# Optimization experiments

Hardware: AMD Instinct MI355X
Metric: run time of the kernel (lower is better)

## Reference

```python
import jax, jax.numpy as jnp
import numpy as np


def _proj(W, b, x):
    # 1x1 conv == per-pixel GEMM over channels: [O,C] x [B,C,H,W] -> [B,O,H,W]
    return jnp.einsum('oc,bchw->bohw', W, x) + b[None, :, None, None]


def _cross(src, ctx, Wq, bq, Wk, bk, Wv, bv):
    # queries from src, keys/values from ctx; returns [B,C,H,W]
    B, C, H, W = src.shape
    HW = H * W
    q = _proj(Wq, bq, src).reshape(B, -1, HW)   # [B, C//8, HW]
    k = _proj(Wk, bk, ctx).reshape(B, -1, HW)   # [B, C//8, HW]
    v = _proj(Wv, bv, ctx).reshape(B, C, HW)    # [B, C,    HW]
    # attn[b,i,j] = softmax_j( q[b,:,i] . k[b,:,j] )
    attn = jax.nn.softmax(jnp.einsum('bci,bcj->bij', q, k), axis=-1)
    out = jnp.einsum('bcj,bij->bci', v, attn)   # [B, C, HW]
    return out.reshape(B, C, H, W)


def setup_inputs() -> dict:
    key = jax.random.key(0)
    ks = jax.random.split(key, 8)
    dim = 256
    B, H, W = 4, 64, 64
    return {
        'x': jax.random.normal(ks[0], (B, dim, H, W), jnp.float32),
        'y': jax.random.normal(ks[1], (B, dim, H, W), jnp.float32),
        'Wq': jax.random.normal(ks[2], (dim // 8, dim), jnp.float32) * 0.05,
        'bq': jax.random.normal(ks[3], (dim // 8,), jnp.float32) * 0.05,
        'Wk': jax.random.normal(ks[4], (dim // 8, dim), jnp.float32) * 0.05,
        'bk': jax.random.normal(ks[5], (dim // 8,), jnp.float32) * 0.05,
        'Wv': jax.random.normal(ks[6], (dim, dim), jnp.float32) * 0.05,
        'bv': jax.random.normal(ks[7], (dim,), jnp.float32) * 0.05,
    }


def reference(x, y, Wq, bq, Wk, bk, Wv, bv):
    outx = _cross(x, y, Wq, bq, Wk, bk, Wv, bv)  # x queries attend to y
    outy = _cross(y, x, Wq, bq, Wk, bk, Wv, bv)  # y queries attend to x
    return (outx, outy)
```

## Files before the change

### kernel.cpp

```cpp
#include <hip/hip_runtime.h>

#define BB 4
#define CC 256
#define DD 32
#define SS 4096

typedef __bf16 bf16;
typedef __bf16 bf16x8 __attribute__((ext_vector_type(8)));
typedef __bf16 bf16x4 __attribute__((ext_vector_type(4)));
typedef float f32x4 __attribute__((ext_vector_type(4)));
typedef unsigned int u32;
typedef u32 u32x4 __attribute__((ext_vector_type(4)));
typedef unsigned short u16;

#define Q_OFF  0
#define K_OFF  1048576
#define V_OFF  2097152
#define WB_OFF 10485760
#define CH_ELEM 16384

static __device__ __forceinline__ u32 pack2(float lo, float hi) {
    bf16 a = (bf16)lo, b = (bf16)hi;
    u16 ua = __builtin_bit_cast(u16, a), ub = __builtin_bit_cast(u16, b);
    return (u32)ua | ((u32)ub << 16);
}

static __device__ __forceinline__ void bar_lds() {
    asm volatile("s_waitcnt lgkmcnt(0)" ::: "memory");
    __builtin_amdgcn_s_barrier();
    asm volatile("" ::: "memory");
}

static __device__ __forceinline__ void bar_vm12() {
    asm volatile("s_waitcnt vmcnt(12)" ::: "memory");
    __builtin_amdgcn_s_barrier();
    asm volatile("" ::: "memory");
}
static __device__ __forceinline__ void bar_plain() {
    asm volatile("" ::: "memory");
    __builtin_amdgcn_s_barrier();
    asm volatile("" ::: "memory");
}

__global__ __launch_bounds__(256) void convert_w_kernel(
    const float* __restrict__ Wq, const float* __restrict__ Wk,
    const float* __restrict__ Wv, bf16* __restrict__ wb)
{
    const int gid = blockIdx.x*256 + threadIdx.x;
    const int idx = gid*8;
    const int o = idx >> 8, cc = idx & 255;
    const float* row = (o < 32) ? (Wq + (size_t)o*CC)
                     : (o < 64) ? (Wk + (size_t)(o-32)*CC)
                                : (Wv + (size_t)(o-64)*CC);
    const float4 a = *(const float4*)(row + cc);
    const float4 c = *(const float4*)(row + cc + 4);
    bf16x8 pk;
    pk[0]=(bf16)a.x; pk[1]=(bf16)a.y; pk[2]=(bf16)a.z; pk[3]=(bf16)a.w;
    pk[4]=(bf16)c.x; pk[5]=(bf16)c.y; pk[6]=(bf16)c.z; pk[7]=(bf16)c.w;
    *(bf16x8*)(wb + idx) = pk;
}

__global__ __launch_bounds__(256, 2) void proj_all_kernel(
    const float* __restrict__ x, const float* __restrict__ y,
    const bf16* __restrict__ wb,
    const float* __restrict__ bq, const float* __restrict__ bk,
    const float* __restrict__ bv,
    bf16* __restrict__ qout, bf16* __restrict__ kout, bf16* __restrict__ vout)
{
    __shared__ __align__(16) char smem[2*5120];
    bf16* xT  = (bf16*)smem;
    u32*  xTw = (u32*)smem;

    const int t    = threadIdx.x;
    const int lane = t & 63;
    const int w    = t >> 6;
    const int ln   = lane & 15;
    const int quad = lane >> 4;

    const int bid  = blockIdx.x;
    const int dirb = bid & 7;
    const int src  = dirb >> 2;
    const int b    = dirb & 3;
    const int i0   = (bid >> 3) * 64;
    const float* in = src ? y : x;
    const float* xbase = in + (size_t)b*CC*SS + i0;

    const int cp = t >> 4;
    const int pq = (t & 15) * 4;

    float bias[5];
    #pragma unroll
    for (int nbl = 0; nbl < 5; ++nbl) {
        const int o = 80*w + nbl*16 + ln;
        bias[nbl] = (o < 32) ? bq[o] : (o < 64) ? bk[o-32] : bv[o-64];
    }
    f32x4 acc[4][5];
    #pragma unroll
    for (int mb = 0; mb < 4; ++mb)
        #pragma unroll
        for (int nbl = 0; nbl < 5; ++nbl)
            acc[mb][nbl] = (f32x4){bias[nbl], bias[nbl], bias[nbl], bias[nbl]};

    const bf16* wrow = wb + (size_t)(80*w + ln)*CC + quad*8;
    bf16x8 bf[5];
    #pragma unroll
    for (int nbl = 0; nbl < 5; ++nbl)
        bf[nbl] = *(const bf16x8*)(wrow + (size_t)nbl*16*CC);

    {
        const float* r0 = xbase + (size_t)(2*cp)*SS + pq;
        const float4 a0 = *(const float4*)r0;
        const float4 a1 = *(const float4*)(r0 + SS);
        xTw[(pq+0)*20 + cp] = pack2(a0.x, a1.x);
        xTw[(pq+1)*20 + cp] = pack2(a0.y, a1.y);
        xTw[(pq+2)*20 + cp] = pack2(a0.z, a1.z);
        xTw[(pq+3)*20 + cp] = pack2(a0.w, a1.w);
    }
    float4 a0, a1;
    {
        const float* r1 = xbase + (size_t)(32 + 2*cp)*SS + pq;
        a0 = *(const float4*)r1;
        a1 = *(const float4*)(r1 + SS);
    }
    bar_lds();

    for (int n = 0; n < 8; ++n) {
        bf16x8 af[4];
        #pragma unroll
        for (int mb = 0; mb < 4; ++mb)
            af[mb] = *(const bf16x8*)(xT + (n&1)*2560 + (mb*16 + ln)*40 + quad*8);
        if (n < 7) {
            u32* dst = xTw + ((n+1)&1)*1280;
            dst[(pq+0)*20 + cp] = pack2(a0.x, a1.x);
            dst[(pq+1)*20 + cp] = pack2(a0.y, a1.y);
            dst[(pq+2)*20 + cp] = pack2(a0.z, a1.z);
            dst[(pq+3)*20 + cp] = pack2(a0.w, a1.w);
        }
        {
            const int cc2 = ((n+2)*32) & 255;
            const float* r2 = xbase + (size_t)(cc2 + 2*cp)*SS + pq;
            a0 = *(const float4*)r2;
            a1 = *(const float4*)(r2 + SS);
        }
        #pragma unroll
        for (int mb = 0; mb < 4; ++mb)
            #pragma unroll
            for (int nbl = 0; nbl < 5; ++nbl)
                acc[mb][nbl] = __builtin_amdgcn_mfma_f32_16x16x32_bf16(
                                   af[mb], bf[nbl], acc[mb][nbl], 0, 0, 0);
        const int ccn = ((n+1)*32) & 255;
        #pragma unroll
        for (int nbl = 0; nbl < 5; ++nbl)
            bf[nbl] = *(const bf16x8*)(wrow + (size_t)nbl*16*CC + ccn);
        bar_lds();
    }

    bf16* qo = qout + (size_t)(src*BB + b)*SS*DD;
    bf16* ko = kout + (size_t)(src*BB + b)*SS*DD;
    bf16* vo = vout + (size_t)(src*BB + b)*CC*SS;
    const int n0 = i0 >> 6;
    #pragma unroll
    for (int nbl = 0; nbl < 5; ++nbl) {
        const int o = 80*w + nbl*16 + ln;
        if (o < 32) {
            #pragma unroll
            for (int mb = 0; mb < 4; ++mb)
                #pragma unroll
                for (int r = 0; r < 4; ++r)
                    qo[(size_t)(i0 + mb*16 + quad*4 + r)*DD + o] = (bf16)acc[mb][nbl][r];
        } else if (o < 64) {
            #pragma unroll
            for (int mb = 0; mb < 4; ++mb)
                #pragma unroll
                for (int r = 0; r < 4; ++r)
                    ko[(size_t)(i0 + mb*16 + quad*4 + r)*DD + (o-32)] = (bf16)acc[mb][nbl][r];
        } else {
            const int c = o - 64;
            const int cb = c >> 4, cl = c & 15;
            #pragma unroll
            for (int mb = 0; mb < 4; ++mb) {
                bf16x4 pk;
                #pragma unroll
                for (int r = 0; r < 4; ++r) pk[r] = (bf16)acc[mb][nbl][r];
                *(bf16x4*)(vo + (size_t)(2*n0 + (mb>>1))*8192 + cb*512
                              + (quad*16 + cl)*8 + (mb&1)*4) = pk;
            }
        }
    }
}

#define L2E   1.4426950408889634f
#define SM_C  (16.0f * L2E)

__global__ __launch_bounds__(256, 2) void attn_kernel(
    const bf16* __restrict__ qg, const bf16* __restrict__ kg,
    const bf16* __restrict__ vg, float* __restrict__ out)
{
    __shared__ __align__(16) char vsm[2*32768];

    const int t    = threadIdx.x;
    const int lane = t & 63;
    const int w    = t >> 6;
    const int ln   = lane & 15;
    const int quad = lane >> 4;

    const int bid  = blockIdx.x;
    const int dirb = bid & 7;
    const int dir  = dirb >> 2;
    const int b    = dirb & 3;
    const int i0   = (bid >> 3) * 64;

    const bf16* q = qg + ((size_t)dir*BB + b)*SS*DD;
    const bf16* k = kg + ((size_t)(1-dir)*BB + b)*SS*DD;
    const bf16* v = vg + ((size_t)(1-dir)*BB + b)*(size_t)CC*SS;
    float* op = out + ((size_t)dir*BB + b)*(size_t)CC*SS;

    const bf16x8 bq = *(const bf16x8*)(q + (size_t)(i0 + w*16 + ln)*DD + quad*8);
    const bf16* kbase = k + (size_t)ln*DD + quad*8;
    const bf16* vstage = v + w*512 + lane*8;
    char* lds0 = vsm + w*1024;

    f32x4 o[16];
    #pragma unroll
    for (int cb = 0; cb < 16; ++cb) o[cb] = (f32x4){0.f,0.f,0.f,0.f};
    f32x4 lpq = (f32x4){0.f,0.f,0.f,0.f};

    bf16x8 kf[4];
    #pragma unroll
    for (int nb = 0; nb < 4; ++nb)
        kf[nb] = *(const bf16x8*)(kbase + (size_t)(nb*16)*DD);

    #define STAGE(ch, buf) do {                                               \
        const bf16* gp_ = vstage + (size_t)(ch)*CH_ELEM;                      \
        char* lp_ = lds0 + (buf)*32768;                                       \
        _Pragma("unroll")                                                     \
        for (int j = 0; j < 8; ++j)                                           \
            __builtin_amdgcn_global_load_lds(                                 \
                (const __attribute__((address_space(1))) void*)(gp_ + j*2048),\
                (__attribute__((address_space(3))) void*)(lp_ + j*4096),      \
                16, 0, 0);                                                    \
    } while (0)

    #define SMAX(sarr, pa) do {                                               \
        float e_[4][4];                                                       \
        _Pragma("unroll")                                                     \
        for (int nb = 0; nb < 4; ++nb)                                        \
            _Pragma("unroll")                                                 \
            for (int r = 0; r < 4; ++r) {                                     \
                e_[nb][r] = exp2f((sarr)[nb][r]*L2E - SM_C);                   \
                lpq[r] += e_[nb][r];                                          \
            }                                                                 \
        _Pragma("unroll")                                                     \
        for (int ks = 0; ks < 2; ++ks) {                                      \
            u32x4 pk_;                                                        \
            _Pragma("unroll")                                                 \
            for (int jp = 0; jp < 4; ++jp)                                    \
                pk_[jp] = pack2(e_[2*ks + (jp>>1)][2*(jp&1)],                 \
                                e_[2*ks + (jp>>1)][2*(jp&1) + 1]);            \
            (pa)[ks] = __builtin_bit_cast(bf16x8, pk_);                       \
        }                                                                     \
    } while (0)

    bf16x8 paA[2], paB[2];
    {
        f32x4 s[4];
        #pragma unroll
        for (int nb = 0; nb < 4; ++nb)
            s[nb] = __builtin_amdgcn_mfma_f32_16x16x32_bf16(
                        kf[nb], bq, (f32x4){0.f,0.f,0.f,0.f}, 0, 0, 0);
        STAGE(0, 0);
        STAGE(1, 1);
        #pragma unroll
        for (int nb = 0; nb < 4; ++nb)
            kf[nb] = *(const bf16x8*)(kbase + (size_t)(64 + nb*16)*DD);
        SMAX(s, paA);
    }

    for (int n = 0; n < 64; ++n) {
        if (n < 63) {
            f32x4 s[4];
            #pragma unroll
            for (int nb = 0; nb < 4; ++nb)
                s[nb] = __builtin_amdgcn_mfma_f32_16x16x32_bf16(
                            kf[nb], bq, (f32x4){0.f,0.f,0.f,0.f}, 0, 0, 0);
            const int j2 = ((n + 2) & 63) * 64;
            #pragma unroll
            for (int nb = 0; nb < 4; ++nb)
                kf[nb] = *(const bf16x8*)(kbase + (size_t)(j2 + nb*16)*DD);
            SMAX(s, paB);
        }

        bar_vm12();

        const char* bufp = vsm + (n & 1)*32768;
        __builtin_amdgcn_s_setprio(1);
        #pragma unroll
        for (int st = 0; st < 32; ++st) {
            const int cb = st & 15;
            const bf16x8 vfr = *(const bf16x8*)(bufp + st*1024 + lane*16);
            o[cb] = __builtin_amdgcn_mfma_f32_16x16x32_bf16(
                        paA[st >> 4], vfr, o[cb], 0, 0, 0);
        }
        __builtin_amdgcn_s_setprio(0);

        bar_plain();
        STAGE((n + 2) & 63, n & 1);

        paA[0] = paB[0];
        paA[1] = paB[1];
    }

    float lp = (lpq[0] + lpq[1]) + (lpq[2] + lpq[3]);
    lp += __shfl_xor(lp, 16);
    lp += __shfl_xor(lp, 32);
    f32x4 ri;
    #pragma unroll
    for (int r = 0; r < 4; ++r)
        ri[r] = 1.0f / __shfl(lp, quad*4 + r);

    #pragma unroll
    for (int cb = 0; cb < 16; ++cb) {
        const int c = cb*16 + ln;
        float4 val = make_float4(o[cb][0]*ri[0], o[cb][1]*ri[1],
                                 o[cb][2]*ri[2], o[cb][3]*ri[3]);
        *(float4*)(op + (size_t)c*SS + i0 + w*16 + quad*4) = val;
    }
    #undef STAGE
    #undef SMAX
}

extern "C" void kernel_launch(void* const* d_in, const int* in_sizes, int n_in,
                              void* d_out, int out_size, void* d_ws, size_t ws_size,
                              hipStream_t stream)
{
    const float* x  = (const float*)d_in[0];
    const float* y  = (const float*)d_in[1];
    const float* Wq = (const float*)d_in[2];
    const float* bq = (const float*)d_in[3];
    const float* Wk = (const float*)d_in[4];
    const float* bk = (const float*)d_in[5];
    const float* Wv = (const float*)d_in[6];
    const float* bv = (const float*)d_in[7];
    float* out = (float*)d_out;
    bf16* ws   = (bf16*)d_ws;

    bf16* qw = ws + Q_OFF;
    bf16* kw = ws + K_OFF;
    bf16* vw = ws + V_OFF;
    bf16* wb = ws + WB_OFF;

    convert_w_kernel<<<40,  256, 0, stream>>>(Wq, Wk, Wv, wb);
    proj_all_kernel <<<512, 256, 0, stream>>>(x, y, wb, bq, bk, bv, qw, kw, vw);
    attn_kernel     <<<512, 256, 0, stream>>>(qw, kw, vw, out);
}
```

Before: 207.2 us.

## Split attention waves by key half so QK/softmax overlaps PV across waves

```diff
diff --git a/kernel.cpp b/kernel.cpp
--- a/kernel.cpp
+++ b/kernel.cpp
@@ -197,6 +197,7 @@
     const bf16* __restrict__ vg, float* __restrict__ out)
 {
     __shared__ __align__(16) char vsm[2*32768];
+    __shared__ float l_s[2][64];
 
     const int t    = threadIdx.x;
     const int lane = t & 63;
@@ -209,26 +210,33 @@
     const int dir  = dirb >> 2;
     const int b    = dirb & 3;
     const int i0   = (bid >> 3) * 64;
+    const int qh   = w >> 1;
+    const int kh   = (w ^ bid) & 1;
 
     const bf16* q = qg + ((size_t)dir*BB + b)*SS*DD;
     const bf16* k = kg + ((size_t)(1-dir)*BB + b)*SS*DD;
     const bf16* v = vg + ((size_t)(1-dir)*BB + b)*(size_t)CC*SS;
     float* op = out + ((size_t)dir*BB + b)*(size_t)CC*SS;
 
-    const bf16x8 bq = *(const bf16x8*)(q + (size_t)(i0 + w*16 + ln)*DD + quad*8);
+    const bf16x8 bq0 = *(const bf16x8*)(q + (size_t)(i0 + qh*32 +      ln)*DD + quad*8);
+    const bf16x8 bq1 = *(const bf16x8*)(q + (size_t)(i0 + qh*32 + 16 + ln)*DD + quad*8);
     const bf16* kbase = k + (size_t)ln*DD + quad*8;
     const bf16* vstage = v + w*512 + lane*8;
     char* lds0 = vsm + w*1024;
 
-    f32x4 o[16];
-    #pragma unroll
-    for (int cb = 0; cb < 16; ++cb) o[cb] = (f32x4){0.f,0.f,0.f,0.f};
-    f32x4 lpq = (f32x4){0.f,0.f,0.f,0.f};
+    f32x4 o0[16], o1[16];
+    #pragma unroll
+    for (int cb = 0; cb < 16; ++cb) {
+        o0[cb] = (f32x4){0.f,0.f,0.f,0.f};
+        o1[cb] = (f32x4){0.f,0.f,0.f,0.f};
+    }
+    f32x4 lpq0 = (f32x4){0.f,0.f,0.f,0.f};
+    f32x4 lpq1 = (f32x4){0.f,0.f,0.f,0.f};
 
     bf16x8 kf[4];
     #pragma unroll
     for (int nb = 0; nb < 4; ++nb)
-        kf[nb] = *(const bf16x8*)(kbase + (size_t)(nb*16)*DD);
+        kf[nb] = *(const bf16x8*)(kbase + (size_t)(kh*64 + nb*16)*DD);
 
     #define STAGE(ch, buf) do {                                               \
         const bf16* gp_ = vstage + (size_t)(ch)*CH_ELEM;                      \
@@ -241,92 +249,138 @@
                 16, 0, 0);                                                    \
     } while (0)
 
-    #define SMAX(sarr, pa) do {                                               \
-        float e_[4][4];                                                       \
+    #define SMAX2(g) do {                                                     \
+        float e0_[4][4], e1_[4][4];                                           \
         _Pragma("unroll")                                                     \
         for (int nb = 0; nb < 4; ++nb)                                        \
             _Pragma("unroll")                                                 \
             for (int r = 0; r < 4; ++r) {                                     \
-                e_[nb][r] = exp2f((sarr)[nb][r]*L2E - SM_C);                   \
-                lpq[r] += e_[nb][r];                                          \
+                e0_[nb][r] = exp2f(s0[nb][r]*L2E - SM_C);                      \
+                e1_[nb][r] = exp2f(s1[nb][r]*L2E - SM_C);                      \
+                lpq0[r] = fmaf((g), e0_[nb][r], lpq0[r]);                     \
+                lpq1[r] = fmaf((g), e1_[nb][r], lpq1[r]);                     \
             }                                                                 \
         _Pragma("unroll")                                                     \
         for (int ks = 0; ks < 2; ++ks) {                                      \
-            u32x4 pk_;                                                        \
+            u32x4 p0_, p1_;                                                   \
             _Pragma("unroll")                                                 \
-            for (int jp = 0; jp < 4; ++jp)                                    \
-                pk_[jp] = pack2(e_[2*ks + (jp>>1)][2*(jp&1)],                 \
-                                e_[2*ks + (jp>>1)][2*(jp&1) + 1]);            \
-            (pa)[ks] = __builtin_bit_cast(bf16x8, pk_);                       \
+            for (int jp = 0; jp < 4; ++jp) {                                  \
+                p0_[jp] = pack2(e0_[2*ks + (jp>>1)][2*(jp&1)],                \
+                                e0_[2*ks + (jp>>1)][2*(jp&1) + 1]);           \
+                p1_[jp] = pack2(e1_[2*ks + (jp>>1)][2*(jp&1)],                \
+                                e1_[2*ks + (jp>>1)][2*(jp&1) + 1]);           \
+            }                                                                 \
+            pa0[ks] = __builtin_bit_cast(bf16x8, p0_);                        \
+            pa1[ks] = __builtin_bit_cast(bf16x8, p1_);                        \
         }                                                                     \
     } while (0)
 
-    bf16x8 paA[2], paB[2];
-    {
-        f32x4 s[4];
+    bf16x8 pa0[2], pa1[2];
+    STAGE(0, 0);
+    STAGE(1, 1);
+    if (kh == 0) {
+        f32x4 s0[4], s1[4];
+        #pragma unroll
+        for (int nb = 0; nb < 4; ++nb) {
+            s0[nb] = __builtin_amdgcn_mfma_f32_16x16x32_bf16(
+                         kf[nb], bq0, (f32x4){0.f,0.f,0.f,0.f}, 0, 0, 0);
+            s1[nb] = __builtin_amdgcn_mfma_f32_16x16x32_bf16(
+                         kf[nb], bq1, (f32x4){0.f,0.f,0.f,0.f}, 0, 0, 0);
+        }
         #pragma unroll
         for (int nb = 0; nb < 4; ++nb)
-            s[nb] = __builtin_amdgcn_mfma_f32_16x16x32_bf16(
-                        kf[nb], bq, (f32x4){0.f,0.f,0.f,0.f}, 0, 0, 0);
-        STAGE(0, 0);
-        STAGE(1, 1);
-        #pragma unroll
-        for (int nb = 0; nb < 4; ++nb)
-            kf[nb] = *(const bf16x8*)(kbase + (size_t)(64 + nb*16)*DD);
-        SMAX(s, paA);
+            kf[nb] = *(const bf16x8*)(kbase + (size_t)(128 + nb*16)*DD);
+        SMAX2(1.0f);
     }
 
     for (int n = 0; n < 64; ++n) {
-        if (n < 63) {
-            f32x4 s[4];
+        bar_vm12();
+        if ((n & 1) == kh) {
+            const char* bufp = vsm + (n & 1)*32768;
+            __builtin_amdgcn_s_setprio(1);
+            #pragma unroll
+            for (int st = 0; st < 32; ++st) {
+                const int cb = st & 15;
+                const bf16x8 vfr = *(const bf16x8*)(bufp + st*1024 + lane*16);
+                o0[cb] = __builtin_amdgcn_mfma_f32_16x16x32_bf16(
+                             pa0[st >> 4], vfr, o0[cb], 0, 0, 0);
+                o1[cb] = __builtin_amdgcn_mfma_f32_16x16x32_bf16(
+                             pa1[st >> 4], vfr, o1[cb], 0, 0, 0);
+            }
+            __builtin_amdgcn_s_setprio(0);
+        } else {
+            f32x4 s0[4], s1[4];
+            #pragma unroll
+            for (int nb = 0; nb < 4; ++nb) {
+                s0[nb] = __builtin_amdgcn_mfma_f32_16x16x32_bf16(
+                             kf[nb], bq0, (f32x4){0.f,0.f,0.f,0.f}, 0, 0, 0);
+                s1[nb] = __builtin_amdgcn_mfma_f32_16x16x32_bf16(
+                             kf[nb], bq1, (f32x4){0.f,0.f,0.f,0.f}, 0, 0, 0);
+            }
+            const int j3 = ((n + 3) & 63) * 64;
             #pragma unroll
             for (int nb = 0; nb < 4; ++nb)
-                s[nb] = __builtin_amdgcn_mfma_f32_16x16x32_bf16(
-                            kf[nb], bq, (f32x4){0.f,0.f,0.f,0.f}, 0, 0, 0);
-            const int j2 = ((n + 2) & 63) * 64;
-            #pragma unroll
-            for (int nb = 0; nb < 4; ++nb)
-                kf[nb] = *(const bf16x8*)(kbase + (size_t)(j2 + nb*16)*DD);
-            SMAX(s, paB);
-        }
-
-        bar_vm12();
-
-        const char* bufp = vsm + (n & 1)*32768;
-        __builtin_amdgcn_s_setprio(1);
-        #pragma unroll
-        for (int st = 0; st < 32; ++st) {
-            const int cb = st & 15;
-            const bf16x8 vfr = *(const bf16x8*)(bufp + st*1024 + lane*16);
-            o[cb] = __builtin_amdgcn_mfma_f32_16x16x32_bf16(
-                        paA[st >> 4], vfr, o[cb], 0, 0, 0);
-        }
-        __builtin_amdgcn_s_setprio(0);
-
+                kf[nb] = *(const bf16x8*)(kbase + (size_t)(j3 + nb*16)*DD);
+            const float g = (n < 63) ? 1.0f : 0.0f;
+            SMAX2(g);
+        }
         bar_plain();
         STAGE((n + 2) & 63, n & 1);
-
-        paA[0] = paB[0];
-        paA[1] = paB[1];
-    }
-
-    float lp = (lpq[0] + lpq[1]) + (lpq[2] + lpq[3]);
-    lp += __shfl_xor(lp, 16);
-    lp += __shfl_xor(lp, 32);
-    f32x4 ri;
-    #pragma unroll
-    for (int r = 0; r < 4; ++r)
-        ri[r] = 1.0f / __shfl(lp, quad*4 + r);
-
-    #pragma unroll
-    for (int cb = 0; cb < 16; ++cb) {
-        const int c = cb*16 + ln;
-        float4 val = make_float4(o[cb][0]*ri[0], o[cb][1]*ri[1],
-                                 o[cb][2]*ri[2], o[cb][3]*ri[3]);
-        *(float4*)(op + (size_t)c*SS + i0 + w*16 + quad*4) = val;
+    }
+
+    asm volatile("s_waitcnt vmcnt(0)" ::: "memory");
+    __builtin_amdgcn_s_barrier();
+
+    float lp0 = (lpq0[0] + lpq0[1]) + (lpq0[2] + lpq0[3]);
+    float lp1 = (lpq1[0] + lpq1[1]) + (lpq1[2] + lpq1[3]);
+    lp0 += __shfl_xor(lp0, 16); lp0 += __shfl_xor(lp0, 32);
+    lp1 += __shfl_xor(lp1, 16); lp1 += __shfl_xor(lp1, 32);
+    if (quad == 0) {
+        l_s[kh][qh*32 +      ln] = lp0;
+        l_s[kh][qh*32 + 16 + ln] = lp1;
+    }
+
+    float* o_s = (float*)vsm;
+    #pragma unroll
+    for (int ph = 0; ph < 2; ++ph) {
+        if (kh == 0 && qh == ph) {
+            #pragma unroll
+            for (int cb = 0; cb < 16; ++cb) {
+                const int c = cb*16 + ln;
+                #pragma unroll
+                for (int r = 0; r < 4; ++r) {
+                    o_s[(quad*4 + r)*257 + c]      = o0[cb][r];
+                    o_s[(16 + quad*4 + r)*257 + c] = o1[cb][r];
+                }
+            }
+        }
+        bar_lds();
+        if (kh == 1 && qh == ph) {
+            #pragma unroll
+            for (int qb = 0; qb < 2; ++qb) {
+                const int q0 = qh*32 + qb*16 + quad*4;
+                f32x4 ri;
+                #pragma unroll
+                for (int r = 0; r < 4; ++r)
+                    ri[r] = 1.0f / (l_s[0][q0 + r] + l_s[1][q0 + r]);
+                #pragma unroll
+                for (int cb = 0; cb < 16; ++cb) {
+                    const int c = cb*16 + ln;
+                    const int row = qb*16 + quad*4;
+                    const f32x4 mine = qb ? o1[cb] : o0[cb];
+                    float4 val;
+                    val.x = (mine[0] + o_s[(row+0)*257 + c]) * ri[0];
+                    val.y = (mine[1] + o_s[(row+1)*257 + c]) * ri[1];
+                    val.z = (mine[2] + o_s[(row+2)*257 + c]) * ri[2];
+                    val.w = (mine[3] + o_s[(row+3)*257 + c]) * ri[3];
+                    *(float4*)(op + (size_t)c*SS + i0 + q0) = val;
+                }
+            }
+        }
+        bar_lds();
     }
     #undef STAGE
-    #undef SMAX
+    #undef SMAX2
 }
 
 extern "C" void kernel_launch(void* const* d_in, const int* in_sizes, int n_in,
```

New measurement: 234.8 us. 1.13x slower.

## Pre-transpose inputs to bf16 tiles and stage them into LDS with direct loads

Applied to the files above, without the earlier changes.

```diff
diff --git a/kernel.cpp b/kernel.cpp
--- a/kernel.cpp
+++ b/kernel.cpp
@@ -23,12 +23,6 @@
     bf16 a = (bf16)lo, b = (bf16)hi;
     u16 ua = __builtin_bit_cast(u16, a), ub = __builtin_bit_cast(u16, b);
     return (u32)ua | ((u32)ub << 16);
-}
-
-static __device__ __forceinline__ void bar_lds() {
-    asm volatile("s_waitcnt lgkmcnt(0)" ::: "memory");
-    __builtin_amdgcn_s_barrier();
-    asm volatile("" ::: "memory");
 }
 
 static __device__ __forceinline__ void bar_vm12() {
@@ -60,16 +54,50 @@
     *(bf16x8*)(wb + idx) = pk;
 }
 
+__global__ __launch_bounds__(256) void transpose_x_kernel(
+    const float* __restrict__ x, const float* __restrict__ y,
+    bf16* __restrict__ xb)
+{
+    const int t    = threadIdx.x;
+    const int bid  = blockIdx.x;
+    const int dirb = bid & 7;
+    const int src  = dirb >> 2;
+    const int b    = dirb & 3;
+    const int tile = bid >> 3;
+    const float* in = (src ? y : x) + (size_t)b*CC*SS;
+    bf16* outp = xb + (size_t)dirb*1048576 + (size_t)tile*CH_ELEM;
+
+    const int pg = t & 15;
+    const int cg = t >> 4;
+    #pragma unroll
+    for (int outer = 0; outer < 2; ++outer) {
+        const int cc0 = outer*128 + cg*8;
+        float4 v4[8];
+        #pragma unroll
+        for (int j = 0; j < 8; ++j)
+            v4[j] = *(const float4*)(in + (size_t)(cc0 + j)*SS + tile*64 + pg*4);
+        #pragma unroll
+        for (int p = 0; p < 4; ++p) {
+            const int pos = pg*4 + p;
+            bf16x8 pk;
+            #pragma unroll
+            for (int j = 0; j < 8; ++j) {
+                const float fv = (p==0)?v4[j].x:(p==1)?v4[j].y:(p==2)?v4[j].z:v4[j].w;
+                pk[j] = (bf16)fv;
+            }
+            *(bf16x8*)(outp + (pos>>4)*4096 + (cc0>>5)*512
+                       + ((cc0>>3)&3)*128 + (pos&15)*8) = pk;
+        }
+    }
+}
+
 __global__ __launch_bounds__(256, 2) void proj_all_kernel(
-    const float* __restrict__ x, const float* __restrict__ y,
-    const bf16* __restrict__ wb,
+    const bf16* __restrict__ xb, const bf16* __restrict__ wb,
     const float* __restrict__ bq, const float* __restrict__ bk,
     const float* __restrict__ bv,
     bf16* __restrict__ qout, bf16* __restrict__ kout, bf16* __restrict__ vout)
 {
-    __shared__ __align__(16) char smem[2*5120];
-    bf16* xT  = (bf16*)smem;
-    u32*  xTw = (u32*)smem;
+    __shared__ __align__(16) char xsm[32768];
 
     const int t    = threadIdx.x;
     const int lane = t & 63;
@@ -81,12 +109,20 @@
     const int dirb = bid & 7;
     const int src  = dirb >> 2;
     const int b    = dirb & 3;
-    const int i0   = (bid >> 3) * 64;
-    const float* in = src ? y : x;
-    const float* xbase = in + (size_t)b*CC*SS + i0;
-
-    const int cp = t >> 4;
-    const int pq = (t & 15) * 4;
+    const int tile = bid >> 3;
+    const int i0   = tile * 64;
+
+    {
+        const bf16* xstage = xb + (size_t)dirb*1048576 + (size_t)tile*CH_ELEM
+                             + w*512 + lane*8;
+        char* ldsb = xsm + w*1024;
+        #pragma unroll
+        for (int j = 0; j < 8; ++j)
+            __builtin_amdgcn_global_load_lds(
+                (const __attribute__((address_space(1))) void*)(xstage + j*2048),
+                (__attribute__((address_space(3))) void*)(ldsb + j*4096),
+                16, 0, 0);
+    }
 
     float bias[5];
     #pragma unroll
@@ -94,6 +130,12 @@
         const int o = 80*w + nbl*16 + ln;
         bias[nbl] = (o < 32) ? bq[o] : (o < 64) ? bk[o-32] : bv[o-64];
     }
+    const bf16* wrow = wb + (size_t)(80*w + ln)*CC + quad*8;
+    bf16x8 bf[5];
+    #pragma unroll
+    for (int nbl = 0; nbl < 5; ++nbl)
+        bf[nbl] = *(const bf16x8*)(wrow + (size_t)nbl*16*CC);
+
     f32x4 acc[4][5];
     #pragma unroll
     for (int mb = 0; mb < 4; ++mb)
@@ -101,47 +143,13 @@
         for (int nbl = 0; nbl < 5; ++nbl)
             acc[mb][nbl] = (f32x4){bias[nbl], bias[nbl], bias[nbl], bias[nbl]};
 
-    const bf16* wrow = wb + (size_t)(80*w + ln)*CC + quad*8;
-    bf16x8 bf[5];
-    #pragma unroll
-    for (int nbl = 0; nbl < 5; ++nbl)
-        bf[nbl] = *(const bf16x8*)(wrow + (size_t)nbl*16*CC);
-
-    {
-        const float* r0 = xbase + (size_t)(2*cp)*SS + pq;
-        const float4 a0 = *(const float4*)r0;
-        const float4 a1 = *(const float4*)(r0 + SS);
-        xTw[(pq+0)*20 + cp] = pack2(a0.x, a1.x);
-        xTw[(pq+1)*20 + cp] = pack2(a0.y, a1.y);
-        xTw[(pq+2)*20 + cp] = pack2(a0.z, a1.z);
-        xTw[(pq+3)*20 + cp] = pack2(a0.w, a1.w);
-    }
-    float4 a0, a1;
-    {
-        const float* r1 = xbase + (size_t)(32 + 2*cp)*SS + pq;
-        a0 = *(const float4*)r1;
-        a1 = *(const float4*)(r1 + SS);
-    }
-    bar_lds();
+    __syncthreads();
 
     for (int n = 0; n < 8; ++n) {
         bf16x8 af[4];
         #pragma unroll
         for (int mb = 0; mb < 4; ++mb)
-            af[mb] = *(const bf16x8*)(xT + (n&1)*2560 + (mb*16 + ln)*40 + quad*8);
-        if (n < 7) {
-            u32* dst = xTw + ((n+1)&1)*1280;
-            dst[(pq+0)*20 + cp] = pack2(a0.x, a1.x);
-            dst[(pq+1)*20 + cp] = pack2(a0.y, a1.y);
-            dst[(pq+2)*20 + cp] = pack2(a0.z, a1.z);
-            dst[(pq+3)*20 + cp] = pack2(a0.w, a1.w);
-        }
-        {
-            const int cc2 = ((n+2)*32) & 255;
-            const float* r2 = xbase + (size_t)(cc2 + 2*cp)*SS + pq;
-            a0 = *(const float4*)r2;
-            a1 = *(const float4*)(r2 + SS);
-        }
+            af[mb] = *(const bf16x8*)(xsm + mb*8192 + n*1024 + lane*16);
         #pragma unroll
         for (int mb = 0; mb < 4; ++mb)
             #pragma unroll
@@ -152,13 +160,12 @@
         #pragma unroll
         for (int nbl = 0; nbl < 5; ++nbl)
             bf[nbl] = *(const bf16x8*)(wrow + (size_t)nbl*16*CC + ccn);
-        bar_lds();
     }
 
     bf16* qo = qout + (size_t)(src*BB + b)*SS*DD;
     bf16* ko = kout + (size_t)(src*BB + b)*SS*DD;
     bf16* vo = vout + (size_t)(src*BB + b)*CC*SS;
-    const int n0 = i0 >> 6;
+    const int n0 = tile;
     #pragma unroll
     for (int nbl = 0; nbl < 5; ++nbl) {
         const int o = 80*w + nbl*16 + ln;
@@ -349,7 +356,8 @@
     bf16* vw = ws + V_OFF;
     bf16* wb = ws + WB_OFF;
 
-    convert_w_kernel<<<40,  256, 0, stream>>>(Wq, Wk, Wv, wb);
-    proj_all_kernel <<<512, 256, 0, stream>>>(x, y, wb, bq, bk, bv, qw, kw, vw);
-    attn_kernel     <<<512, 256, 0, stream>>>(qw, kw, vw, out);
-}
+    convert_w_kernel  <<<40,  256, 0, stream>>>(Wq, Wk, Wv, wb);
+    transpose_x_kernel<<<512, 256, 0, stream>>>(x, y, vw);
+    proj_all_kernel   <<<512, 256, 0, stream>>>(vw, wb, bq, bk, bv, qw, kw, vw);
+    attn_kernel       <<<512, 256, 0, stream>>>(qw, kw, vw, out);
+}
```

After: 222.8 us. 7.5% more time.
